# Kernel tuning notes

Hardware: AMD Instinct MI355X
Metric: run time of the kernel (lower is better)

## Reference

```python
import jax, jax.numpy as jnp
import numpy as np

L_SIDE = 32
N_PIX = 12 * L_SIDE * L_SIDE      # 12288 sphere pixels
N_VALID = N_PIX // 2              # theta <= pi/2 hemisphere (first half by construction)
A_TH, B_TH, C_TH = 0.03, 1.0, 1.0  # ellipsoid semi-axes (thickness, 1, 1)


def _sphere_angles(n):
    # Deterministic Fibonacci-lattice sphere sampling standing in for SphereHealpix.
    i = np.arange(n, dtype=np.float64)
    z = 1.0 - 2.0 * (i + 0.5) / n          # cos(theta), descending -> theta<=pi/2 iff i < n/2
    theta = np.arccos(z)
    phi = (i * np.pi * (3.0 - np.sqrt(5.0))) % (2.0 * np.pi)
    return theta.astype(np.float32), phi.astype(np.float32)


def _ellipse_valid():
    # Faithful translation of ReconstructionModel.ellipse_valid for the valid hemisphere.
    theta_all, phi_all = _sphere_angles(N_PIX)
    tv = theta_all[:N_VALID].astype(np.float32)
    pv = phi_all[:N_VALID].astype(np.float32)
    a, b, c = np.float32(A_TH), np.float32(B_TH), np.float32(C_TH)
    # cartesian coords of valid pixels (computed BEFORE the angle shift)
    xv = np.cos(pv) * np.sin(tv)
    yv = np.sin(pv) * np.sin(tv)
    # meshgrid(phi, x) / meshgrid(theta, y) with ij indexing -> angles vary on rows, coords on cols
    phi = ((pv + np.pi / 2) % (2 * np.pi)).astype(np.float32)[:, None]   # [Nv,1]
    theta = ((tv + np.pi / 2) % np.pi).astype(np.float32)[:, None]       # [Nv,1]
    x = xv[None, :]
    y = yv[None, :]
    x_c = np.sin(2 * theta) / 2 * np.cos(phi)
    y_c = -np.sin(2 * theta) / 2 * np.sin(phi)
    z_c = (np.cos(2 * theta) + 1) / 2
    r = np.sqrt(2 * (np.cos(2 * theta) + 1)) / 2 + np.float32(1e-5)
    a2, b2, c2 = a * a, b * b, c * c
    ct, st = np.cos(theta), np.sin(theta)
    cp, sp = np.cos(phi), np.sin(phi)
    ct2, ct4 = ct ** 2, ct ** 4
    cp2 = cp ** 2
    x2, y2 = x ** 2, y ** 2
    s2p = np.sin(2.0 * phi)
    with np.errstate(invalid='ignore'):
        S = (-b2 * ct2 + b2 * ct4 - b2 * y2 - c2 * x2
             + a2 * b2 * ct4 + b2 * c2 * ct2 - b2 * c2 * ct4
             - b2 * x2 * cp2 + b2 * y2 * cp2 + c2 * x2 * cp2 - c2 * y2 * cp2
             - a2 * x2 * ct2 + c2 * x2 * ct2
             + b2 * x * y * s2p - c2 * x * y * s2p
             + a2 * x2 * cp2 * ct2 - a2 * y2 * cp2 * ct2
             - c2 * x2 * cp2 * ct2 + c2 * y2 * cp2 * ct2
             + 2.0 * b2 * x * cp * ct * st - 2.0 * b2 * y * ct * sp * st
             + 2.0 * c2 * x * y * cp * ct2 * sp - 2.0 * a2 * x * y * cp * ct2 * sp)
        num = (a * c * np.sqrt(S)
               - a2 * b * ct2 + 2.0 * a2 * b * ct4
               + 2.0 * b * c2 * ct2 - 2.0 * b * c2 * ct4
               + a2 * b * x * cp * ct * st - b * c2 * x * cp * ct * st
               - a2 * b * y * ct * sp * st + b * c2 * y * ct * sp * st)
        den = b * (a2 * ct2 - c2 * ct2 + c2)
        z = num / den
        f = ((x - x_c) ** 2 + (y - y_c) ** 2 + (z - z_c) ** 2) / r ** 2
    f = np.where(np.isnan(f), np.float32(0.0), f)   # f[f != f] = 0
    return f.astype(np.float32)


def setup_inputs() -> dict:
    key = jax.random.key(0)
    x = jax.random.uniform(key, (8, 16, N_PIX), dtype=jnp.float32)
    all_responses = jnp.asarray(_ellipse_valid())   # [N_VALID, N_VALID]
    return {"x": x, "all_responses": all_responses}


def reference(x, all_responses):
    nv = all_responses.shape[0]
    # masked gather: theta <= pi/2 is exactly the first nv pixels by construction
    x_valid = x[:, :, :nv]                                   # [B,C,Nv]
    mixture = jnp.einsum('bcn,nm->bcm', x_valid, all_responses)
    mixture = jnp.clip(mixture, 0.0, 1.0)                    # mix='clip'
    # masked scatter back into zero buffer
    out = jnp.zeros_like(x).at[:, :, :nv].set(mixture)
    return out
```

## Files before the change

kernel.cpp:

```cpp
#include <hip/hip_runtime.h>
#include <hip/hip_bf16.h>


#define NPIX 12288
#define NV   6144
#define MR   128
#define BNW  32
#define KST  128
#define NSTR (NV / BNW)
#define PARTF ((size_t)MR * NV)

typedef __attribute__((ext_vector_type(8))) short bf16x8;
typedef __attribute__((ext_vector_type(4))) float f32x4;
typedef __attribute__((ext_vector_type(4))) unsigned u32x4;

__device__ __forceinline__ unsigned pk2(float lo, float hi) {
    __hip_bfloat162 h = __float22bfloat162_rn(make_float2(lo, hi));
    union { __hip_bfloat162 h; unsigned u; } v; v.h = h; return v.u;
}

__device__ __forceinline__ bf16x8 cvt8(f32x4 a, f32x4 b) {
    union { unsigned u[4]; bf16x8 v; } r;
    r.u[0] = pk2(a[0], a[1]); r.u[1] = pk2(a[2], a[3]);
    r.u[2] = pk2(b[0], b[1]); r.u[3] = pk2(b[2], b[3]);
    return r.v;
}

__global__ __launch_bounds__(256) void prep_kernel(const float* __restrict__ x,
                                                   unsigned short* __restrict__ abf) {
    int q = blockIdx.x * 256 + threadIdx.x;
    int m = q / (NV / 8);
    int r = q % (NV / 8);
    int k = r * 8;
    const float* src = x + (size_t)m * NPIX + k;
    f32x4 a = *(const f32x4*)(src);
    f32x4 b = *(const f32x4*)(src + 4);
    u32x4 o;
    o[0] = pk2(a[0], a[1]); o[1] = pk2(a[2], a[3]);
    o[2] = pk2(b[0], b[1]); o[3] = pk2(b[2], b[3]);
    *(u32x4*)(abf + (size_t)m * NV + k) = o;
}

__device__ __forceinline__ void sload(const float*& bptr, float2 (&r)[8]) {
    #pragma unroll
    for (int gi = 0; gi < 4; ++gi) {
        const float* p = bptr + (size_t)(gi * 32) * NV;
        r[2 * gi]     = *(const float2*)(p);
        r[2 * gi + 1] = *(const float2*)(p + NV);
    }
    bptr += (size_t)KST * NV;
}

__device__ __forceinline__ void wstage(unsigned char* buf, const float2 (&r)[8],
                                       int kq, int nq, int sw0, int sw1) {
    #pragma unroll
    for (int gi = 0; gi < 4; ++gi) {
        unsigned lo = pk2(r[2 * gi].x, r[2 * gi + 1].x);
        unsigned hi = pk2(r[2 * gi].y, r[2 * gi + 1].y);
        const int kbyte = (kq + gi * 32) * 2;
        *(unsigned*)(buf + nq * 256       + (kbyte ^ sw0)) = lo;
        *(unsigned*)(buf + (nq + 1) * 256 + (kbyte ^ sw1)) = hi;
    }
}

template<bool BF16A>
__device__ __forceinline__ void compute_step(const unsigned char* buf,
        const unsigned short* __restrict__ A, const float* __restrict__ X,
        size_t arow0, size_t arow1, int ln, int lg, f32x4 (&acc)[2][2]) {
    bf16x8 afr[2][4];
    #pragma unroll
    for (int ks = 0; ks < 4; ++ks) {
        if (BF16A) {
            afr[0][ks] = *(const bf16x8*)(A + arow0 + ks * 32);
            afr[1][ks] = *(const bf16x8*)(A + arow1 + ks * 32);
        } else {
            f32x4 p0 = *(const f32x4*)(X + arow0 + ks * 32);
            f32x4 p1 = *(const f32x4*)(X + arow0 + ks * 32 + 4);
            afr[0][ks] = cvt8(p0, p1);
            f32x4 q0 = *(const f32x4*)(X + arow1 + ks * 32);
            f32x4 q1 = *(const f32x4*)(X + arow1 + ks * 32 + 4);
            afr[1][ks] = cvt8(q0, q1);
        }
    }
    const int swn = (ln & 7) << 4;
    #pragma unroll
    for (int nt = 0; nt < 2; ++nt) {
        const int rowb = (nt * 16 + ln) * 256;
        #pragma unroll
        for (int ks = 0; ks < 4; ++ks) {
            bf16x8 bfr = *(const bf16x8*)(buf + rowb + (((lg * 16) + ks * 64) ^ swn));
            acc[0][nt] = __builtin_amdgcn_mfma_f32_16x16x32_bf16(afr[0][ks], bfr, acc[0][nt], 0, 0, 0);
            acc[1][nt] = __builtin_amdgcn_mfma_f32_16x16x32_bf16(afr[1][ks], bfr, acc[1][nt], 0, 0, 0);
        }
    }
}

template<bool BF16A>
__global__ __launch_bounds__(256, 2) void gemm_kernel(const float* __restrict__ X,
        const unsigned short* __restrict__ A, const float* __restrict__ R,
        float* __restrict__ out, float* __restrict__ wpart,
        int nchunks, int kch) {
    __shared__ unsigned char Bs0[32 * 256];
    __shared__ unsigned char Bs1[32 * 256];

    const int tid = threadIdx.x;
    const int w = tid >> 6;
    const int l = tid & 63;
    const int ln = l & 15, lg = l >> 4;
    const int chunk = blockIdx.x / NSTR;
    const int nb = blockIdx.x % NSTR;
    const int n0 = nb * BNW;
    const int kbase = chunk * kch;
    const int nsi = kch / KST;

    const int kq = (tid >> 4) * 2;
    const int nq = (tid & 15) * 2;
    const float* bptr = R + (size_t)(kbase + kq) * NV + (n0 + nq);
    const int sw0 = (nq & 7) << 4;
    const int sw1 = ((nq + 1) & 7) << 4;

    size_t arow0, arow1;
    if (BF16A) {
        arow0 = (size_t)(w * 32 + ln) * NV + kbase + lg * 8;
        arow1 = arow0 + (size_t)16 * NV;
    } else {
        arow0 = (size_t)(w * 32 + ln) * NPIX + kbase + lg * 8;
        arow1 = arow0 + (size_t)16 * NPIX;
    }

    f32x4 acc[2][2];
    #pragma unroll
    for (int a = 0; a < 2; ++a)
        #pragma unroll
        for (int b = 0; b < 2; ++b) {
            acc[a][b][0] = 0.f; acc[a][b][1] = 0.f;
            acc[a][b][2] = 0.f; acc[a][b][3] = 0.f;
        }

    float2 ring0[8], ring1[8];
    sload(bptr, ring0);
    sload(bptr, ring1);
    wstage(Bs0, ring0, kq, nq, sw0, sw1);
    __syncthreads();

    #pragma unroll 1
    for (int it = 0; it < nsi / 2; ++it) {
        const int s = it * 2;
        if (s + 2 < nsi) sload(bptr, ring0);
        compute_step<BF16A>(Bs0, A, X, arow0, arow1, ln, lg, acc);
        arow0 += KST; arow1 += KST;
        wstage(Bs1, ring1, kq, nq, sw0, sw1);
        __syncthreads();
        if (s + 3 < nsi) sload(bptr, ring1);
        compute_step<BF16A>(Bs1, A, X, arow0, arow1, ln, lg, acc);
        arow0 += KST; arow1 += KST;
        if (s + 2 < nsi) wstage(Bs0, ring0, kq, nq, sw0, sw1);
        __syncthreads();
    }

    float* dst;
    size_t rstride;
    if (chunk < 2) { dst = out + (size_t)chunk * NV; rstride = NPIX; }
    else           { dst = wpart + (size_t)(chunk - 2) * PARTF; rstride = NV; }
    #pragma unroll
    for (int mt = 0; mt < 2; ++mt) {
        const int mbase = w * 32 + mt * 16 + lg * 4;
        #pragma unroll
        for (int nt = 0; nt < 2; ++nt) {
            const size_t cb = (size_t)(n0 + nt * 16 + ln);
            #pragma unroll
            for (int j = 0; j < 4; ++j)
                dst[(size_t)(mbase + j) * rstride + cb] = acc[mt][nt][j];
        }
    }
}

__global__ __launch_bounds__(256) void reduce_kernel(float* __restrict__ out,
        const float* __restrict__ wpart, int nextra) {
    int q = blockIdx.x * 256 + threadIdx.x;
    int m = q / (NV / 4);
    int r = q % (NV / 4);
    size_t base = (size_t)m * NPIX + r * 4;
    f32x4 a = *(f32x4*)(out + base);
    f32x4 b = *(f32x4*)(out + base + NV);
    #pragma unroll
    for (int i = 0; i < 4; ++i) a[i] += b[i];
    #pragma unroll 1
    for (int p = 0; p < nextra; ++p) {
        f32x4 c = *(const f32x4*)(wpart + (size_t)p * PARTF + (size_t)m * NV + r * 4);
        #pragma unroll
        for (int i = 0; i < 4; ++i) a[i] += c[i];
    }
    f32x4 cz, z;
    #pragma unroll
    for (int i = 0; i < 4; ++i) {
        cz[i] = fminf(fmaxf(a[i], 0.f), 1.f);
        z[i] = 0.f;
    }
    *(f32x4*)(out + base) = cz;
    *(f32x4*)(out + base + NV) = z;
}

extern "C" void kernel_launch(void* const* d_in, const int* in_sizes, int n_in,
                              void* d_out, int out_size, void* d_ws, size_t ws_size,
                              hipStream_t stream) {
    const float* x = (const float*)d_in[0];
    const float* R = (const float*)d_in[1];
    float* out = (float*)d_out;

    const size_t abytes = (size_t)MR * NV * 2;
    const bool use_ws = ws_size >= abytes;
    int chunks = 2;
    float* wpart = nullptr;
    if (use_ws) {
        size_t rem = ws_size - abytes;
        if      (rem >= 6 * PARTF * 4) chunks = 8;
        else if (rem >= 2 * PARTF * 4) chunks = 4;
        wpart = (float*)((char*)d_ws + abytes);
    }
    const int kch = NV / chunks;

    if (use_ws) {
        unsigned short* abf = (unsigned short*)d_ws;
        prep_kernel<<<(MR * NV / 8) / 256, 256, 0, stream>>>(x, abf);
        gemm_kernel<true><<<NSTR * chunks, 256, 0, stream>>>(x, abf, R, out, wpart, chunks, kch);
    } else {
        gemm_kernel<false><<<NSTR * chunks, 256, 0, stream>>>(x, nullptr, R, out, wpart, chunks, kch);
    }
    reduce_kernel<<<(MR * NV / 4) / 256, 256, 0, stream>>>(out, wpart, chunks - 2);
}
```

Before: 247.8 us.

## Pre-transpose responses to bf16 and stream tiles directly into LDS

Adds a transpose kernel that converts the fp32 response matrix into a bf16 transposed copy in workspace. A new GEMM kernel then loads B tiles with global_load_lds straight into swizzled shared memory, with a fixed 8-way K split. This removes the per-tile fp32 to bf16 conversion and the register staging from the GEMM. In exchange it adds a full extra pass that reads the large matrix and writes half of it again, and it needs a much larger workspace. If the workspace is too small, the code falls back to a 2-chunk path.

After: 278.6 us. 1.12x slower.

```diff
diff --git a/kernel.cpp b/kernel.cpp
--- a/kernel.cpp
+++ b/kernel.cpp
@@ -19,11 +19,10 @@
     union { __hip_bfloat162 h; unsigned u; } v; v.h = h; return v.u;
 }
 
-__device__ __forceinline__ bf16x8 cvt8(f32x4 a, f32x4 b) {
-    union { unsigned u[4]; bf16x8 v; } r;
-    r.u[0] = pk2(a[0], a[1]); r.u[1] = pk2(a[2], a[3]);
-    r.u[2] = pk2(b[0], b[1]); r.u[3] = pk2(b[2], b[3]);
-    return r.v;
+__device__ __forceinline__ void gld16(const void* g, void* l) {
+    __builtin_amdgcn_global_load_lds(
+        (const __attribute__((address_space(1))) void*)g,
+        (__attribute__((address_space(3))) void*)l, 16, 0, 0);
 }
 
 __global__ __launch_bounds__(256) void prep_kernel(const float* __restrict__ x,
@@ -41,6 +40,128 @@
     *(u32x4*)(abf + (size_t)m * NV + k) = o;
 }
 
+__global__ __launch_bounds__(256) void trans_kernel(const float* __restrict__ R,
+                                                    unsigned short* __restrict__ RT) {
+    __shared__ float T[64][65];
+    const int tid = threadIdx.x;
+    const int kt = blockIdx.x % (NV / 64);
+    const int nt = blockIdx.x / (NV / 64);
+    const int k0 = kt * 64, n0 = nt * 64;
+    const int colg = (tid & 15) * 4;
+    const int rowb = tid >> 4;
+    #pragma unroll
+    for (int it = 0; it < 4; ++it) {
+        const int row = it * 16 + rowb;
+        f32x4 v = *(const f32x4*)(R + (size_t)(k0 + row) * NV + n0 + colg);
+        #pragma unroll
+        for (int j = 0; j < 4; ++j) T[colg + j][row] = v[j];
+    }
+    __syncthreads();
+    const int n = tid >> 2, seg = tid & 3;
+    float f[16];
+    #pragma unroll
+    for (int u = 0; u < 16; ++u) f[u] = T[n][seg * 16 + u];
+    u32x4 o0, o1;
+    o0[0] = pk2(f[0], f[1]);  o0[1] = pk2(f[2], f[3]);
+    o0[2] = pk2(f[4], f[5]);  o0[3] = pk2(f[6], f[7]);
+    o1[0] = pk2(f[8], f[9]);  o1[1] = pk2(f[10], f[11]);
+    o1[2] = pk2(f[12], f[13]); o1[3] = pk2(f[14], f[15]);
+    unsigned short* dst = RT + (size_t)(n0 + n) * NV + k0 + seg * 16;
+    *(u32x4*)(dst) = o0;
+    *(u32x4*)(dst + 8) = o1;
+}
+
+__global__ __launch_bounds__(256) void gemm2_kernel(
+        const unsigned short* __restrict__ A,
+        const unsigned short* __restrict__ RT,
+        float* __restrict__ out, float* __restrict__ wpart) {
+    __shared__ unsigned char Bs[2][8192];
+
+    const int tid = threadIdx.x;
+    const int w = tid >> 6, l = tid & 63;
+    const int ln = l & 15, lg = l >> 4;
+    const int chunk = blockIdx.x & 7;
+    const int nb = blockIdx.x >> 3;
+    const int n0 = nb * BNW;
+    const int kbase = chunk * 768;
+    const int nsi = 768 / KST;
+
+    const int f0 = tid * 16, f1 = 4096 + tid * 16;
+    const int n_0 = f0 >> 8, n_1 = f1 >> 8;
+    const int ko0 = (f0 & 255) ^ ((n_0 & 7) << 4);
+    const int ko1 = (f1 & 255) ^ ((n_1 & 7) << 4);
+    const char* g0 = (const char*)(RT + (size_t)(n0 + n_0) * NV + kbase) + ko0;
+    const char* g1 = (const char*)(RT + (size_t)(n0 + n_1) * NV + kbase) + ko1;
+
+    size_t arow0 = (size_t)(w * 32 + ln) * NV + kbase + lg * 8;
+    size_t arow1 = arow0 + (size_t)16 * NV;
+
+    f32x4 acc[2][2];
+    #pragma unroll
+    for (int a = 0; a < 2; ++a)
+        #pragma unroll
+        for (int b = 0; b < 2; ++b) {
+            acc[a][b][0] = 0.f; acc[a][b][1] = 0.f;
+            acc[a][b][2] = 0.f; acc[a][b][3] = 0.f;
+        }
+
+    gld16(g0, &Bs[0][f0]);
+    gld16(g1, &Bs[0][f1]);
+    __syncthreads();
+
+    const int swn = (ln & 7) << 4;
+    #pragma unroll 1
+    for (int t = 0; t < nsi; ++t) {
+        if (t + 1 < nsi) {
+            const int nb2 = (t + 1) & 1;
+            gld16(g0 + (t + 1) * 256, &Bs[nb2][f0]);
+            gld16(g1 + (t + 1) * 256, &Bs[nb2][f1]);
+        }
+        const unsigned char* buf = Bs[t & 1];
+        bf16x8 afr[2][4];
+        #pragma unroll
+        for (int ks = 0; ks < 4; ++ks) {
+            afr[0][ks] = *(const bf16x8*)(A + arow0 + ks * 32);
+            afr[1][ks] = *(const bf16x8*)(A + arow1 + ks * 32);
+        }
+        #pragma unroll
+        for (int nt = 0; nt < 2; ++nt) {
+            const int rowb = (nt * 16 + ln) * 256;
+            #pragma unroll
+            for (int ks = 0; ks < 4; ++ks) {
+                bf16x8 bfr = *(const bf16x8*)(buf + rowb + (((lg * 16) + ks * 64) ^ swn));
+                acc[0][nt] = __builtin_amdgcn_mfma_f32_16x16x32_bf16(afr[0][ks], bfr, acc[0][nt], 0, 0, 0);
+                acc[1][nt] = __builtin_amdgcn_mfma_f32_16x16x32_bf16(afr[1][ks], bfr, acc[1][nt], 0, 0, 0);
+            }
+        }
+        arow0 += KST; arow1 += KST;
+        __syncthreads();
+    }
+
+    float* dst;
+    size_t rstride;
+    if (chunk < 2) { dst = out + (size_t)chunk * NV; rstride = NPIX; }
+    else           { dst = wpart + (size_t)(chunk - 2) * PARTF; rstride = NV; }
+    #pragma unroll
+    for (int mt = 0; mt < 2; ++mt) {
+        const int mbase = w * 32 + mt * 16 + lg * 4;
+        #pragma unroll
+        for (int nt = 0; nt < 2; ++nt) {
+            const size_t cb = (size_t)(n0 + nt * 16 + ln);
+            #pragma unroll
+            for (int j = 0; j < 4; ++j)
+                dst[(size_t)(mbase + j) * rstride + cb] = acc[mt][nt][j];
+        }
+    }
+}
+
+__device__ __forceinline__ bf16x8 cvt8(f32x4 a, f32x4 b) {
+    union { unsigned u[4]; bf16x8 v; } r;
+    r.u[0] = pk2(a[0], a[1]); r.u[1] = pk2(a[2], a[3]);
+    r.u[2] = pk2(b[0], b[1]); r.u[3] = pk2(b[2], b[3]);
+    return r.v;
+}
+
 __device__ __forceinline__ void sload(const float*& bptr, float2 (&r)[8]) {
     #pragma unroll
     for (int gi = 0; gi < 4; ++gi) {
@@ -63,24 +184,18 @@
     }
 }
 
-template<bool BF16A>
-__device__ __forceinline__ void compute_step(const unsigned char* buf,
-        const unsigned short* __restrict__ A, const float* __restrict__ X,
-        size_t arow0, size_t arow1, int ln, int lg, f32x4 (&acc)[2][2]) {
+__device__ __forceinline__ void compute_fb(const unsigned char* buf,
+        const float* __restrict__ X, size_t arow0, size_t arow1,
+        int ln, int lg, f32x4 (&acc)[2][2]) {
     bf16x8 afr[2][4];
     #pragma unroll
     for (int ks = 0; ks < 4; ++ks) {
-        if (BF16A) {
-            afr[0][ks] = *(const bf16x8*)(A + arow0 + ks * 32);
-            afr[1][ks] = *(const bf16x8*)(A + arow1 + ks * 32);
-        } else {
-            f32x4 p0 = *(const f32x4*)(X + arow0 + ks * 32);
-            f32x4 p1 = *(const f32x4*)(X + arow0 + ks * 32 + 4);
-            afr[0][ks] = cvt8(p0, p1);
-            f32x4 q0 = *(const f32x4*)(X + arow1 + ks * 32);
-            f32x4 q1 = *(const f32x4*)(X + arow1 + ks * 32 + 4);
-            afr[1][ks] = cvt8(q0, q1);
-        }
+        f32x4 p0 = *(const f32x4*)(X + arow0 + ks * 32);
+        f32x4 p1 = *(const f32x4*)(X + arow0 + ks * 32 + 4);
+        afr[0][ks] = cvt8(p0, p1);
+        f32x4 q0 = *(const f32x4*)(X + arow1 + ks * 32);
+        f32x4 q1 = *(const f32x4*)(X + arow1 + ks * 32 + 4);
+        afr[1][ks] = cvt8(q0, q1);
     }
     const int swn = (ln & 7) << 4;
     #pragma unroll
@@ -95,39 +210,25 @@
     }
 }
 
-template<bool BF16A>
-__global__ __launch_bounds__(256, 2) void gemm_kernel(const float* __restrict__ X,
-        const unsigned short* __restrict__ A, const float* __restrict__ R,
-        float* __restrict__ out, float* __restrict__ wpart,
-        int nchunks, int kch) {
+__global__ __launch_bounds__(256) void gemm_fb_kernel(const float* __restrict__ X,
+        const float* __restrict__ R, float* __restrict__ out) {
     __shared__ unsigned char Bs0[32 * 256];
     __shared__ unsigned char Bs1[32 * 256];
-
     const int tid = threadIdx.x;
-    const int w = tid >> 6;
-    const int l = tid & 63;
+    const int w = tid >> 6, l = tid & 63;
     const int ln = l & 15, lg = l >> 4;
     const int chunk = blockIdx.x / NSTR;
     const int nb = blockIdx.x % NSTR;
     const int n0 = nb * BNW;
-    const int kbase = chunk * kch;
-    const int nsi = kch / KST;
-
+    const int kbase = chunk * (NV / 2);
+    const int nsi = (NV / 2) / KST;
     const int kq = (tid >> 4) * 2;
     const int nq = (tid & 15) * 2;
     const float* bptr = R + (size_t)(kbase + kq) * NV + (n0 + nq);
     const int sw0 = (nq & 7) << 4;
     const int sw1 = ((nq + 1) & 7) << 4;
-
-    size_t arow0, arow1;
-    if (BF16A) {
-        arow0 = (size_t)(w * 32 + ln) * NV + kbase + lg * 8;
-        arow1 = arow0 + (size_t)16 * NV;
-    } else {
-        arow0 = (size_t)(w * 32 + ln) * NPIX + kbase + lg * 8;
-        arow1 = arow0 + (size_t)16 * NPIX;
-    }
-
+    size_t arow0 = (size_t)(w * 32 + ln) * NPIX + kbase + lg * 8;
+    size_t arow1 = arow0 + (size_t)16 * NPIX;
     f32x4 acc[2][2];
     #pragma unroll
     for (int a = 0; a < 2; ++a)
@@ -136,32 +237,26 @@
             acc[a][b][0] = 0.f; acc[a][b][1] = 0.f;
             acc[a][b][2] = 0.f; acc[a][b][3] = 0.f;
         }
-
     float2 ring0[8], ring1[8];
     sload(bptr, ring0);
     sload(bptr, ring1);
     wstage(Bs0, ring0, kq, nq, sw0, sw1);
     __syncthreads();
-
     #pragma unroll 1
     for (int it = 0; it < nsi / 2; ++it) {
         const int s = it * 2;
         if (s + 2 < nsi) sload(bptr, ring0);
-        compute_step<BF16A>(Bs0, A, X, arow0, arow1, ln, lg, acc);
+        compute_fb(Bs0, X, arow0, arow1, ln, lg, acc);
         arow0 += KST; arow1 += KST;
         wstage(Bs1, ring1, kq, nq, sw0, sw1);
         __syncthreads();
         if (s + 3 < nsi) sload(bptr, ring1);
-        compute_step<BF16A>(Bs1, A, X, arow0, arow1, ln, lg, acc);
+        compute_fb(Bs1, X, arow0, arow1, ln, lg, acc);
         arow0 += KST; arow1 += KST;
         if (s + 2 < nsi) wstage(Bs0, ring0, kq, nq, sw0, sw1);
         __syncthreads();
     }
-
-    float* dst;
-    size_t rstride;
-    if (chunk < 2) { dst = out + (size_t)chunk * NV; rstride = NPIX; }
-    else           { dst = wpart + (size_t)(chunk - 2) * PARTF; rstride = NV; }
+    float* dst = out + (size_t)chunk * NV;
     #pragma unroll
     for (int mt = 0; mt < 2; ++mt) {
         const int mbase = w * 32 + mt * 16 + lg * 4;
@@ -170,7 +265,7 @@
             const size_t cb = (size_t)(n0 + nt * 16 + ln);
             #pragma unroll
             for (int j = 0; j < 4; ++j)
-                dst[(size_t)(mbase + j) * rstride + cb] = acc[mt][nt][j];
+                dst[(size_t)(mbase + j) * NPIX + cb] = acc[mt][nt][j];
         }
     }
 }
@@ -208,24 +303,20 @@
     const float* R = (const float*)d_in[1];
     float* out = (float*)d_out;
 
-    const size_t abytes = (size_t)MR * NV * 2;
-    const bool use_ws = ws_size >= abytes;
-    int chunks = 2;
-    float* wpart = nullptr;
-    if (use_ws) {
-        size_t rem = ws_size - abytes;
-        if      (rem >= 6 * PARTF * 4) chunks = 8;
-        else if (rem >= 2 * PARTF * 4) chunks = 4;
-        wpart = (float*)((char*)d_ws + abytes);
-    }
-    const int kch = NV / chunks;
-
-    if (use_ws) {
+    const size_t abytes  = (size_t)MR * NV * 2;
+    const size_t rtbytes = (size_t)NV * NV * 2;
+    const size_t pbytes  = 6 * PARTF * 4;
+
+    if (ws_size >= abytes + rtbytes + pbytes) {
         unsigned short* abf = (unsigned short*)d_ws;
+        unsigned short* rt  = (unsigned short*)((char*)d_ws + abytes);
+        float* wpart = (float*)((char*)d_ws + abytes + rtbytes);
         prep_kernel<<<(MR * NV / 8) / 256, 256, 0, stream>>>(x, abf);
-        gemm_kernel<true><<<NSTR * chunks, 256, 0, stream>>>(x, abf, R, out, wpart, chunks, kch);
+        trans_kernel<<<(NV / 64) * (NV / 64), 256, 0, stream>>>(R, rt);
+        gemm2_kernel<<<NSTR * 8, 256, 0, stream>>>(abf, rt, out, wpart);
+        reduce_kernel<<<(MR * NV / 4) / 256, 256, 0, stream>>>(out, wpart, 6);
     } else {
-        gemm_kernel<false><<<NSTR * chunks, 256, 0, stream>>>(x, nullptr, R, out, wpart, chunks, kch);
-    }
-    reduce_kernel<<<(MR * NV / 4) / 256, 256, 0, stream>>>(out, wpart, chunks - 2);
-}
+        gemm_fb_kernel<<<NSTR * 2, 256, 0, stream>>>(x, R, out);
+        reduce_kernel<<<(MR * NV / 4) / 256, 256, 0, stream>>>(out, nullptr, 0);
+    }
+}
```
